# Optimization experiments

Measured on AMD Instinct MI355X. Metric: run time of the kernel, lower is better.

## Reference

```python
import jax, jax.numpy as jnp
import numpy as np

D = 512      # d_model
H = 8        # nhead
HD = D // H  # head dim
L = 8        # axis-0 length (torch seq dim, batch_first=False)
S = 128      # axis-1 length (torch batch dim; relation-tensor axis)
NL = 3       # encoder layers
EPS = 1e-5


def setup_inputs() -> dict:
    key = jax.random.key(0)
    ks = jax.random.split(key, 16)
    w = lambda k, shape: jax.random.normal(k, shape, jnp.float32) * 0.02
    return {
        "x": jax.random.normal(ks[0], (L, S, D), jnp.float32),
        # stacked per-layer transformer params (leading dim = NL)
        "attn_in_w": w(ks[1], (NL, 3 * D, D)), "attn_in_b": jnp.zeros((NL, 3 * D), jnp.float32),
        "attn_out_w": w(ks[2], (NL, D, D)),    "attn_out_b": jnp.zeros((NL, D), jnp.float32),
        "ln1_w": jnp.ones((NL, D), jnp.float32), "ln1_b": jnp.zeros((NL, D), jnp.float32),
        "ln2_w": jnp.ones((NL, D), jnp.float32), "ln2_b": jnp.zeros((NL, D), jnp.float32),
        "ff1_w": w(ks[3], (NL, 4 * D, D)), "ff1_b": jnp.zeros((NL, 4 * D), jnp.float32),
        "ff2_w": w(ks[4], (NL, D, 4 * D)), "ff2_b": jnp.zeros((NL, D), jnp.float32),
        "fln_w": jnp.ones((D,), jnp.float32), "fln_b": jnp.zeros((D,), jnp.float32),
        # 4 projection MLPs stacked: 0=sub, 1=obj, 2=verb_sub, 3=verb_obj
        "mlp_w0": w(ks[5], (4, D, D)), "mlp_b0": jnp.zeros((4, D), jnp.float32),
        "mlp_w1": w(ks[6], (4, D, D)), "mlp_b1": jnp.zeros((4, D), jnp.float32),
        "mlp_w2": w(ks[7], (4, D, D)), "mlp_b2": jnp.zeros((4, D), jnp.float32),
    }


def _ln(x, w, b):
    m = jnp.mean(x, axis=-1, keepdims=True)
    v = jnp.mean(jnp.square(x - m), axis=-1, keepdims=True)
    return (x - m) * jax.lax.rsqrt(v + EPS) * w + b


def _mha(x, in_w, in_b, out_w, out_b):
    # x: (L, B, D); attention over axis 0 (torch batch_first=False semantics)
    l, b, _ = x.shape
    qkv = x @ in_w.T + in_b                      # (L, B, 3D)
    q, k, v = jnp.split(qkv, 3, axis=-1)
    q = q.reshape(l, b, H, HD)
    k = k.reshape(l, b, H, HD)
    v = v.reshape(l, b, H, HD)
    scores = jnp.einsum("lbhd,mbhd->bhlm", q, k) / jnp.sqrt(jnp.float32(HD))
    attn = jax.nn.softmax(scores, axis=-1)
    o = jnp.einsum("bhlm,mbhd->lbhd", attn, v).reshape(l, b, D)
    return o @ out_w.T + out_b


def _mlp(x, w0, b0, w1, b1, w2, b2):
    h = jax.nn.relu(x @ w0.T + b0)
    h = jax.nn.relu(h @ w1.T + b1)
    return h @ w2.T + b2


def _forward(x, attn_in_w, attn_in_b, attn_out_w, attn_out_b,
             ln1_w, ln1_b, ln2_w, ln2_b, ff1_w, ff1_b, ff2_w, ff2_b,
             fln_w, fln_b, mlp_w0, mlp_b0, mlp_w1, mlp_b1, mlp_w2, mlp_b2):
    # TransformerEncoder (post-norm, relu, no dropout at eval)
    h = x
    for i in range(NL):
        h = _ln(h + _mha(h, attn_in_w[i], attn_in_b[i], attn_out_w[i], attn_out_b[i]),
                ln1_w[i], ln1_b[i])
        ff = jax.nn.relu(h @ ff1_w[i].T + ff1_b[i]) @ ff2_w[i].T + ff2_b[i]
        h = _ln(h + ff, ln2_w[i], ln2_b[i])
    h = _ln(h, fln_w, fln_b)  # final encoder norm

    sub = _mlp(h, mlp_w0[0], mlp_b0[0], mlp_w1[0], mlp_b1[0], mlp_w2[0], mlp_b2[0])
    obj = _mlp(h, mlp_w0[1], mlp_b0[1], mlp_w1[1], mlp_b1[1], mlp_w2[1], mlp_b2[1])
    vsub = _mlp(h, mlp_w0[2], mlp_b0[2], mlp_w1[2], mlp_b1[2], mlp_w2[2], mlp_b2[2])
    vobj = _mlp(h, mlp_w0[3], mlp_b0[3], mlp_w1[3], mlp_b1[3], mlp_w2[3], mlp_b2[3])

    # sub.unsqueeze(1) * vsub.unsqueeze(2): (B0, S, S, D)
    sub4 = sub[:, None, :, :] * vsub[:, :, None, :]
    obj4 = obj[:, None, :, :] * vobj[:, :, None, :]
    # p_x = sub4 @ obj4.transpose(-2, -1): (B0, S, S, S)
    return jnp.einsum("bijd,bikd->bijk", sub4, obj4)


def reference(x, attn_in_w, attn_in_b, attn_out_w, attn_out_b,
              ln1_w, ln1_b, ln2_w, ln2_b, ff1_w, ff1_b, ff2_w, ff2_b,
              fln_w, fln_b, mlp_w0, mlp_b0, mlp_w1, mlp_b1, mlp_w2, mlp_b2):
    return _forward(x, attn_in_w, attn_in_b, attn_out_w, attn_out_b,
                    ln1_w, ln1_b, ln2_w, ln2_b, ff1_w, ff1_b, ff2_w, ff2_b,
                    fln_w, fln_b, mlp_w0, mlp_b0, mlp_w1, mlp_b1, mlp_w2, mlp_b2)
```

## Files before the change

kernel.cpp:

```cpp
#include <hip/hip_runtime.h>
#include <hip/hip_bf16.h>

#define DEV __device__ __forceinline__

typedef __attribute__((ext_vector_type(8))) short bf16x8;
typedef __attribute__((ext_vector_type(8))) unsigned short u16x8;
typedef __attribute__((ext_vector_type(4))) float f32x4;

DEV unsigned short f2bf(float f) {
  return __builtin_bit_cast(unsigned short, __float2bfloat16(f));
}
DEV float bf2f(unsigned short h) { return __uint_as_float(((unsigned int)h) << 16); }

DEV int swz(int row, int byteoff) { return row * 128 + (byteoff ^ ((row & 7) << 4)); }

__global__ void cvt_kernel(const float* __restrict__ src, unsigned short* __restrict__ dst,
                           float* __restrict__ dstf, int n) {
  long i = ((long)blockIdx.x * blockDim.x + threadIdx.x) * 8;
  long stride = (long)gridDim.x * blockDim.x * 8;
  for (; i < n; i += stride) {
    f32x4 a = *(const f32x4*)(src + i);
    f32x4 b = *(const f32x4*)(src + i + 4);
    u16x8 o;
    o[0] = f2bf(a[0]); o[1] = f2bf(a[1]); o[2] = f2bf(a[2]); o[3] = f2bf(a[3]);
    o[4] = f2bf(b[0]); o[5] = f2bf(b[1]); o[6] = f2bf(b[2]); o[7] = f2bf(b[3]);
    *(u16x8*)(dst + i) = o;
    if (dstf) { *(f32x4*)(dstf + i) = a; *(f32x4*)(dstf + i + 4) = b; }
  }
}

struct CvtJobs { const float* s[7]; unsigned short* d[7]; int n[7]; };
__global__ void cvtw_kernel(CvtJobs J) {
  const int seg = blockIdx.y;
  const float* __restrict__ src = J.s[seg];
  unsigned short* __restrict__ dst = J.d[seg];
  const int n = J.n[seg];
  long i = ((long)blockIdx.x * blockDim.x + threadIdx.x) * 8;
  long stride = (long)gridDim.x * blockDim.x * 8;
  for (; i < n; i += stride) {
    f32x4 a = *(const f32x4*)(src + i);
    f32x4 b = *(const f32x4*)(src + i + 4);
    u16x8 o;
    o[0] = f2bf(a[0]); o[1] = f2bf(a[1]); o[2] = f2bf(a[2]); o[3] = f2bf(a[3]);
    o[4] = f2bf(b[0]); o[5] = f2bf(b[1]); o[6] = f2bf(b[2]); o[7] = f2bf(b[3]);
    *(u16x8*)(dst + i) = o;
  }
}

template <int BM, int ACT, int WF32, int WBF>
__global__ __launch_bounds__(256) void gemm_kernel(
    const unsigned short* __restrict__ X, const unsigned short* __restrict__ Wt,
    const float* __restrict__ bias, float* Yf, unsigned short* __restrict__ Ybf,
    int M, int N, int K, long xbs, long wbs, long bbs, long ybs) {
  constexpr int CA = (BM * 64) / (256 * 8);
  constexpr int ABY = BM * 64 * 2;
  constexpr int BBY = 64 * 64 * 2;
  constexpr int MI = BM / 32;
  __shared__ __align__(16) char Asb[2 * ABY];
  __shared__ __align__(16) char Bsb[2 * BBY];
  const int t = threadIdx.x;
  const int bn = blockIdx.x, bm = blockIdx.y, bz = blockIdx.z;
  const unsigned short* Xp = X + (long)bz * xbs;
  const unsigned short* Wp = Wt + (long)bz * wbs;

  const int lane = t & 63, wv = t >> 6;
  const int wr = wv >> 1, wc = wv & 1;
  f32x4 acc[MI][2] = {};

  int rowA[CA], slotA[CA], rowB[2], slotB[2];
#pragma unroll
  for (int c = 0; c < CA; ++c) { int id = c * 256 + t; rowA[c] = id >> 3; slotA[c] = id & 7; }
#pragma unroll
  for (int c = 0; c < 2; ++c) { int id = c * 256 + t; rowB[c] = id >> 3; slotB[c] = id & 7; }

  u16x8 ra[CA], rb[2];
  auto load = [&](int kt) {
#pragma unroll
    for (int c = 0; c < CA; ++c)
      ra[c] = *(const u16x8*)(Xp + (long)(bm * BM + rowA[c]) * K + kt + slotA[c] * 8);
#pragma unroll
    for (int c = 0; c < 2; ++c)
      rb[c] = *(const u16x8*)(Wp + (long)(bn * 64 + rowB[c]) * K + kt + slotB[c] * 8);
  };
  auto store = [&](int cur) {
#pragma unroll
    for (int c = 0; c < CA; ++c)
      *(u16x8*)(Asb + cur * ABY + swz(rowA[c], slotA[c] * 16)) = ra[c];
#pragma unroll
    for (int c = 0; c < 2; ++c)
      *(u16x8*)(Bsb + cur * BBY + swz(rowB[c], slotB[c] * 16)) = rb[c];
  };

  const int NT = K >> 6;
  load(0);
  store(0);
  load(64);
  __syncthreads();
  for (int ki = 0; ki < NT; ++ki) {
    const int cur = ki & 1;
    if (ki + 1 < NT) store(cur ^ 1);
    if (ki + 2 < NT) load((ki + 2) << 6);
#pragma unroll
    for (int kk = 0; kk < 2; ++kk) {
      const int kb = kk * 64 + ((lane >> 4) << 4);
      bf16x8 af[MI], bfv[2];
#pragma unroll
      for (int mi = 0; mi < MI; ++mi)
        af[mi] = *(const bf16x8*)(Asb + cur * ABY + swz(wr * (MI * 16) + mi * 16 + (lane & 15), kb));
#pragma unroll
      for (int ni = 0; ni < 2; ++ni)
        bfv[ni] = *(const bf16x8*)(Bsb + cur * BBY + swz(wc * 32 + ni * 16 + (lane & 15), kb));
#pragma unroll
      for (int mi = 0; mi < MI; ++mi)
#pragma unroll
        for (int ni = 0; ni < 2; ++ni)
          acc[mi][ni] = __builtin_amdgcn_mfma_f32_16x16x32_bf16(af[mi], bfv[ni], acc[mi][ni], 0, 0, 0);
    }
    __syncthreads();
  }
#pragma unroll
  for (int ni = 0; ni < 2; ++ni) {
    const int n = bn * 64 + wc * 32 + ni * 16 + (lane & 15);
    const float bv = bias[(long)bz * bbs + n];
#pragma unroll
    for (int mi = 0; mi < MI; ++mi) {
#pragma unroll
      for (int rr = 0; rr < 4; ++rr) {
        const int gm = bm * BM + wr * (MI * 16) + mi * 16 + ((lane >> 4) << 2) + rr;
        float v = acc[mi][ni][rr] + bv;
        if (ACT == 1) v = fmaxf(v, 0.f);
        const long o = (long)bz * ybs + (long)gm * N + n;
        if (WF32) Yf[o] = v;
        if (WBF) Ybf[o] = f2bf(v);
      }
    }
  }
}

__global__ __launch_bounds__(256) void attn_kernel(const unsigned short* __restrict__ qkv,
                                                   unsigned short* __restrict__ o) {
  __shared__ float P[512];
  const int s = blockIdx.x;
  const int t = threadIdx.x;
#pragma unroll
  for (int rep = 0; rep < 2; ++rep) {
    const int idx = t + rep * 256;
    const int h = idx >> 6, l = (idx >> 3) & 7, m = idx & 7;
    const unsigned short* qp = qkv + (long)(l * 128 + s) * 1536 + h * 64;
    const unsigned short* kp = qkv + (long)(m * 128 + s) * 1536 + 512 + h * 64;
    float acc = 0.f;
#pragma unroll
    for (int c = 0; c < 64; c += 8) {
      u16x8 q8 = *(const u16x8*)(qp + c);
      u16x8 k8 = *(const u16x8*)(kp + c);
#pragma unroll
      for (int j = 0; j < 8; ++j) acc += bf2f(q8[j]) * bf2f(k8[j]);
    }
    P[idx] = acc * 0.125f;
  }
  __syncthreads();
  if (t < 64) {
    const int base = t * 8;
    float mx = -1e30f;
#pragma unroll
    for (int m = 0; m < 8; ++m) mx = fmaxf(mx, P[base + m]);
    float e[8], sum = 0.f;
#pragma unroll
    for (int m = 0; m < 8; ++m) { e[m] = expf(P[base + m] - mx); sum += e[m]; }
    const float inv = 1.f / sum;
#pragma unroll
    for (int m = 0; m < 8; ++m) P[base + m] = e[m] * inv;
  }
  __syncthreads();
#pragma unroll
  for (int rep = 0; rep < 16; ++rep) {
    const int idx = t + rep * 256;
    const int d = idx & 63, h = (idx >> 6) & 7, l = idx >> 9;
    float acc = 0.f;
#pragma unroll
    for (int m = 0; m < 8; ++m)
      acc += P[h * 64 + l * 8 + m] * bf2f(qkv[(long)(m * 128 + s) * 1536 + 1024 + h * 64 + d]);
    o[(long)(l * 128 + s) * 512 + h * 64 + d] = f2bf(acc);
  }
}

template <int RES, int WF32>
__global__ __launch_bounds__(256) void ln_kernel(const float* a, const float* res,
                                                 const float* __restrict__ w,
                                                 const float* __restrict__ bb, float* hf,
                                                 unsigned short* __restrict__ hbf) {
  __shared__ float red[8];
  const int row = blockIdx.x, t = threadIdx.x;
  const long base = (long)row * 512;
  float x0 = a[base + t], x1 = a[base + t + 256];
  if (RES) { x0 += res[base + t]; x1 += res[base + t + 256]; }
  float s = x0 + x1;
#pragma unroll
  for (int msk = 32; msk; msk >>= 1) s += __shfl_xor(s, msk, 64);
  if ((t & 63) == 0) red[t >> 6] = s;
  __syncthreads();
  const float mean = (red[0] + red[1] + red[2] + red[3]) * (1.f / 512.f);
  const float d0 = x0 - mean, d1 = x1 - mean;
  float v = d0 * d0 + d1 * d1;
#pragma unroll
  for (int msk = 32; msk; msk >>= 1) v += __shfl_xor(v, msk, 64);
  if ((t & 63) == 0) red[4 + (t >> 6)] = v;
  __syncthreads();
  const float var = (red[4] + red[5] + red[6] + red[7]) * (1.f / 512.f);
  const float inv = rsqrtf(var + 1e-5f);
  const float o0 = d0 * inv * w[t] + bb[t];
  const float o1 = d1 * inv * w[t + 256] + bb[t + 256];
  if (WF32) { hf[base + t] = o0; hf[base + t + 256] = o1; }
  hbf[base + t] = f2bf(o0);
  hbf[base + t + 256] = f2bf(o1);
}

__global__ __launch_bounds__(256) void phasec_kernel(const float* __restrict__ subp,
                                                     const unsigned short* __restrict__ objbf,
                                                     const float* __restrict__ vsub,
                                                     const float* __restrict__ vobj,
                                                     float* __restrict__ out) {
  constexpr int ABY = 128 * 64 * 2;
  __shared__ __align__(16) char Asb[2 * ABY];
  __shared__ __align__(16) char Bsb[2 * ABY];
  __shared__ float Wl[512];
  const int t = threadIdx.x;
  const int i = blockIdx.x, b = blockIdx.y;
  const long base_bi = ((long)b * 128 + i) * 512;
  for (int d = t; d < 512; d += 256) Wl[d] = vsub[base_bi + d] * vobj[base_bi + d];

  const int lane = t & 63, wv = t >> 6;
  const int wr = wv >> 1, wc = wv & 1;
  f32x4 acc[4][4] = {};

  int row[4], slot[4];
#pragma unroll
  for (int c = 0; c < 4; ++c) { int id = c * 256 + t; row[c] = id >> 3; slot[c] = id & 7; }

  f32x4 fa[4][2];
  u16x8 rb[4];
  auto load = [&](int kt) {
#pragma unroll
    for (int c = 0; c < 4; ++c) {
      const long g = ((long)b * 128 + row[c]) * 512 + kt + slot[c] * 8;
      fa[c][0] = *(const f32x4*)(subp + g);
      fa[c][1] = *(const f32x4*)(subp + g + 4);
      rb[c] = *(const u16x8*)(objbf + g);
    }
  };
  auto store = [&](int cur, int ktd) {
#pragma unroll
    for (int c = 0; c < 4; ++c) {
      const float* wp = Wl + ktd + slot[c] * 8;
      f32x4 w0 = *(const f32x4*)wp;
      f32x4 w1 = *(const f32x4*)(wp + 4);
      u16x8 oa;
      oa[0] = f2bf(fa[c][0][0] * w0[0]); oa[1] = f2bf(fa[c][0][1] * w0[1]);
      oa[2] = f2bf(fa[c][0][2] * w0[2]); oa[3] = f2bf(fa[c][0][3] * w0[3]);
      oa[4] = f2bf(fa[c][1][0] * w1[0]); oa[5] = f2bf(fa[c][1][1] * w1[1]);
      oa[6] = f2bf(fa[c][1][2] * w1[2]); oa[7] = f2bf(fa[c][1][3] * w1[3]);
      *(u16x8*)(Asb + cur * ABY + swz(row[c], slot[c] * 16)) = oa;
      *(u16x8*)(Bsb + cur * ABY + swz(row[c], slot[c] * 16)) = rb[c];
    }
  };

  __syncthreads();
  load(0);
  store(0, 0);
  load(64);
  __syncthreads();
  for (int ki = 0; ki < 8; ++ki) {
    const int cur = ki & 1;
    if (ki + 1 < 8) store(cur ^ 1, (ki + 1) * 64);
    if (ki + 2 < 8) load((ki + 2) * 64);
#pragma unroll
    for (int kk = 0; kk < 2; ++kk) {
      const int kb = kk * 64 + ((lane >> 4) << 4);
      bf16x8 af[4], bfv[4];
#pragma unroll
      for (int mi = 0; mi < 4; ++mi)
        af[mi] = *(const bf16x8*)(Asb + cur * ABY + swz(wr * 64 + mi * 16 + (lane & 15), kb));
#pragma unroll
      for (int ni = 0; ni < 4; ++ni)
        bfv[ni] = *(const bf16x8*)(Bsb + cur * ABY + swz(wc * 64 + ni * 16 + (lane & 15), kb));
#pragma unroll
      for (int mi = 0; mi < 4; ++mi)
#pragma unroll
        for (int ni = 0; ni < 4; ++ni)
          acc[mi][ni] = __builtin_amdgcn_mfma_f32_16x16x32_bf16(af[mi], bfv[ni], acc[mi][ni], 0, 0, 0);
    }
    __syncthreads();
  }
  float* ob = out + ((long)b * 128 + i) * 128 * 128;
#pragma unroll
  for (int mi = 0; mi < 4; ++mi) {
#pragma unroll
    for (int rr = 0; rr < 4; ++rr) {
      const int j = wr * 64 + mi * 16 + ((lane >> 4) << 2) + rr;
      float* orow = ob + (long)j * 128 + wc * 64 + (lane & 15);
#pragma unroll
      for (int ni = 0; ni < 4; ++ni) orow[ni * 16] = acc[mi][ni][rr];
    }
  }
}

extern "C" void kernel_launch(void* const* d_in, const int* in_sizes, int n_in, void* d_out,
                              int out_size, void* d_ws, size_t ws_size, hipStream_t stream) {
  const float* x          = (const float*)d_in[0];
  const float* attn_in_w  = (const float*)d_in[1];
  const float* attn_in_b  = (const float*)d_in[2];
  const float* attn_out_w = (const float*)d_in[3];
  const float* attn_out_b = (const float*)d_in[4];
  const float* ln1_w = (const float*)d_in[5];
  const float* ln1_b = (const float*)d_in[6];
  const float* ln2_w = (const float*)d_in[7];
  const float* ln2_b = (const float*)d_in[8];
  const float* ff1_w = (const float*)d_in[9];
  const float* ff1_b = (const float*)d_in[10];
  const float* ff2_w = (const float*)d_in[11];
  const float* ff2_b = (const float*)d_in[12];
  const float* fln_w = (const float*)d_in[13];
  const float* fln_b = (const float*)d_in[14];
  const float* mlp_w0 = (const float*)d_in[15];
  const float* mlp_b0 = (const float*)d_in[16];
  const float* mlp_w1 = (const float*)d_in[17];
  const float* mlp_b1 = (const float*)d_in[18];
  const float* mlp_w2 = (const float*)d_in[19];
  const float* mlp_b2 = (const float*)d_in[20];
  float* out = (float*)d_out;
  (void)in_sizes; (void)n_in; (void)out_size; (void)ws_size;

  char* ws = (char*)d_ws;
  size_t off = 0;
  auto alloc = [&](size_t bytes) -> void* {
    void* p = (void*)(ws + off);
    off += (bytes + 255) & ~(size_t)255;
    return p;
  };
  unsigned short* wq  = (unsigned short*)alloc((size_t)3 * 1536 * 512 * 2);
  unsigned short* wo  = (unsigned short*)alloc((size_t)3 * 512 * 512 * 2);
  unsigned short* wf1 = (unsigned short*)alloc((size_t)3 * 2048 * 512 * 2);
  unsigned short* wf2 = (unsigned short*)alloc((size_t)3 * 512 * 2048 * 2);
  unsigned short* wm0 = (unsigned short*)alloc((size_t)4 * 512 * 512 * 2);
  unsigned short* wm1 = (unsigned short*)alloc((size_t)4 * 512 * 512 * 2);
  unsigned short* wm2 = (unsigned short*)alloc((size_t)4 * 512 * 512 * 2);
  float* h            = (float*)alloc((size_t)1024 * 512 * 4);
  unsigned short* hbf = (unsigned short*)alloc((size_t)1024 * 512 * 2);
  unsigned short* t1  = (unsigned short*)alloc((size_t)1024 * 2048 * 2);
  float* t2           = (float*)alloc((size_t)1024 * 512 * 4);
  unsigned short* ao  = (unsigned short*)alloc((size_t)1024 * 512 * 2);
  unsigned short* z1  = (unsigned short*)alloc((size_t)4 * 1024 * 512 * 2);
  unsigned short* z2  = (unsigned short*)alloc((size_t)4 * 1024 * 512 * 2);
  float* hf4          = (float*)alloc((size_t)4 * 1024 * 512 * 4);
  unsigned short* hb4 = (unsigned short*)alloc((size_t)4 * 1024 * 512 * 2);

  CvtJobs J;
  J.s[0] = attn_in_w;  J.d[0] = wq;  J.n[0] = 3 * 1536 * 512;
  J.s[1] = attn_out_w; J.d[1] = wo;  J.n[1] = 3 * 512 * 512;
  J.s[2] = ff1_w;      J.d[2] = wf1; J.n[2] = 3 * 2048 * 512;
  J.s[3] = ff2_w;      J.d[3] = wf2; J.n[3] = 3 * 512 * 2048;
  J.s[4] = mlp_w0;     J.d[4] = wm0; J.n[4] = 4 * 512 * 512;
  J.s[5] = mlp_w1;     J.d[5] = wm1; J.n[5] = 4 * 512 * 512;
  J.s[6] = mlp_w2;     J.d[6] = wm2; J.n[6] = 4 * 512 * 512;
  cvtw_kernel<<<dim3(512, 7), 256, 0, stream>>>(J);
  cvt_kernel<<<256, 256, 0, stream>>>(x, hbf, h, 1024 * 512);

  for (int i = 0; i < 3; ++i) {
    gemm_kernel<64, 0, 0, 1><<<dim3(24, 16, 1), 256, 0, stream>>>(
        hbf, wq + (long)i * 1536 * 512, attn_in_b + i * 1536, nullptr, t1, 1024, 1536, 512, 0, 0, 0, 0);
    attn_kernel<<<128, 256, 0, stream>>>(t1, ao);
    gemm_kernel<32, 0, 1, 0><<<dim3(8, 32, 1), 256, 0, stream>>>(
        ao, wo + (long)i * 512 * 512, attn_out_b + i * 512, t2, nullptr, 1024, 512, 512, 0, 0, 0, 0);
    ln_kernel<1, 1><<<1024, 256, 0, stream>>>(t2, h, ln1_w + i * 512, ln1_b + i * 512, h, hbf);
    gemm_kernel<64, 1, 0, 1><<<dim3(32, 16, 1), 256, 0, stream>>>(
        hbf, wf1 + (long)i * 2048 * 512, ff1_b + i * 2048, nullptr, t1, 1024, 2048, 512, 0, 0, 0, 0);
    gemm_kernel<32, 0, 1, 0><<<dim3(8, 32, 1), 256, 0, stream>>>(
        t1, wf2 + (long)i * 512 * 2048, ff2_b + i * 512, t2, nullptr, 1024, 512, 2048, 0, 0, 0, 0);
    ln_kernel<1, 1><<<1024, 256, 0, stream>>>(t2, h, ln2_w + i * 512, ln2_b + i * 512, h, hbf);
  }
  ln_kernel<0, 0><<<1024, 256, 0, stream>>>(h, nullptr, fln_w, fln_b, h, hbf);

  gemm_kernel<32, 1, 0, 1><<<dim3(8, 32, 4), 256, 0, stream>>>(
      hbf, wm0, mlp_b0, nullptr, z1, 1024, 512, 512, 0, 512 * 512, 512, 1024 * 512);
  gemm_kernel<32, 1, 0, 1><<<dim3(8, 32, 4), 256, 0, stream>>>(
      z1, wm1, mlp_b1, nullptr, z2, 1024, 512, 512, 1024 * 512, 512 * 512, 512, 1024 * 512);
  gemm_kernel<32, 0, 1, 1><<<dim3(8, 32, 4), 256, 0, stream>>>(
      z2, wm2, mlp_b2, hf4, hb4, 1024, 512, 512, 1024 * 512, 512 * 512, 512, 1024 * 512);

  phasec_kernel<<<dim3(128, 8), 256, 0, stream>>>(
      hf4, hb4 + 1 * 1024 * 512, hf4 + 2L * 1024 * 512, hf4 + 3L * 1024 * 512, out);
}
```

Baseline: 379.6 us.

## Fuse LayerNorms into GEMM prologue/epilogue via atomic row statistics

Removes the standalone LayerNorm kernels. GEMM epilogues now add the residual, accumulate per-row sum and sum-of-squares with atomics, and the next GEMM applies the normalization while loading its fp32 A tile. The change also widens GEMM tiles to 64x128 for the wide projections, folds the input conversion into the batched weight-convert launch, and stages the phase-C output through LDS for coalesced vector stores. The cost is a single-pass variance (E[x^2]-mean^2) with atomic accumulation, a memset, fp32 A-operand loads, and renormalizing the residual redundantly in epilogues.

```diff
diff --git a/kernel.cpp b/kernel.cpp
--- a/kernel.cpp
+++ b/kernel.cpp
@@ -14,22 +14,7 @@
 
 DEV int swz(int row, int byteoff) { return row * 128 + (byteoff ^ ((row & 7) << 4)); }
 
-__global__ void cvt_kernel(const float* __restrict__ src, unsigned short* __restrict__ dst,
-                           float* __restrict__ dstf, int n) {
-  long i = ((long)blockIdx.x * blockDim.x + threadIdx.x) * 8;
-  long stride = (long)gridDim.x * blockDim.x * 8;
-  for (; i < n; i += stride) {
-    f32x4 a = *(const f32x4*)(src + i);
-    f32x4 b = *(const f32x4*)(src + i + 4);
-    u16x8 o;
-    o[0] = f2bf(a[0]); o[1] = f2bf(a[1]); o[2] = f2bf(a[2]); o[3] = f2bf(a[3]);
-    o[4] = f2bf(b[0]); o[5] = f2bf(b[1]); o[6] = f2bf(b[2]); o[7] = f2bf(b[3]);
-    *(u16x8*)(dst + i) = o;
-    if (dstf) { *(f32x4*)(dstf + i) = a; *(f32x4*)(dstf + i + 4) = b; }
-  }
-}
-
-struct CvtJobs { const float* s[7]; unsigned short* d[7]; int n[7]; };
+struct CvtJobs { const float* s[8]; unsigned short* d[8]; int n[8]; };
 __global__ void cvtw_kernel(CvtJobs J) {
   const int seg = blockIdx.y;
   const float* __restrict__ src = J.s[seg];
@@ -47,91 +32,151 @@
   }
 }
 
-template <int BM, int ACT, int WF32, int WBF>
-__global__ __launch_bounds__(256) void gemm_kernel(
-    const unsigned short* __restrict__ X, const unsigned short* __restrict__ Wt,
-    const float* __restrict__ bias, float* Yf, unsigned short* __restrict__ Ybf,
+template <int BM, int BN, int ALN, int RES, int RLN, int ACT, int STATS, int OUTF32, int OUTBF>
+__global__ __launch_bounds__(256) void gemm2_kernel(
+    const unsigned short* __restrict__ Xb, const float* __restrict__ Xf,
+    const float* __restrict__ sA, const float* __restrict__ gA, const float* __restrict__ bA,
+    const unsigned short* __restrict__ W, const float* __restrict__ bias,
+    const float* __restrict__ resf, const float* __restrict__ sR,
+    const float* __restrict__ gR, const float* __restrict__ bR,
+    float* __restrict__ Yf, unsigned short* __restrict__ Ybf, float* __restrict__ stats,
     int M, int N, int K, long xbs, long wbs, long bbs, long ybs) {
-  constexpr int CA = (BM * 64) / (256 * 8);
-  constexpr int ABY = BM * 64 * 2;
-  constexpr int BBY = 64 * 64 * 2;
-  constexpr int MI = BM / 32;
+  constexpr int CA = BM / 32, CB = BN / 32;
+  constexpr int ABY = BM * 64 * 2, BBY = BN * 64 * 2;
+  constexpr int MI = BM / 32, NI = BN / 32;
   __shared__ __align__(16) char Asb[2 * ABY];
   __shared__ __align__(16) char Bsb[2 * BBY];
   const int t = threadIdx.x;
   const int bn = blockIdx.x, bm = blockIdx.y, bz = blockIdx.z;
-  const unsigned short* Xp = X + (long)bz * xbs;
-  const unsigned short* Wp = Wt + (long)bz * wbs;
-
-  const int lane = t & 63, wv = t >> 6;
-  const int wr = wv >> 1, wc = wv & 1;
-  f32x4 acc[MI][2] = {};
-
-  int rowA[CA], slotA[CA], rowB[2], slotB[2];
+  const int lane = t & 63, wv = t >> 6, wr = wv >> 1, wc = wv & 1;
+
+  int rowA[CA], slotA[CA], rowB[CB], slotB[CB];
 #pragma unroll
   for (int c = 0; c < CA; ++c) { int id = c * 256 + t; rowA[c] = id >> 3; slotA[c] = id & 7; }
 #pragma unroll
-  for (int c = 0; c < 2; ++c) { int id = c * 256 + t; rowB[c] = id >> 3; slotB[c] = id & 7; }
-
-  u16x8 ra[CA], rb[2];
+  for (int c = 0; c < CB; ++c) { int id = c * 256 + t; rowB[c] = id >> 3; slotB[c] = id & 7; }
+
+  float mA[CA], iA[CA];
+  if (ALN) {
+#pragma unroll
+    for (int c = 0; c < CA; ++c) {
+      const int gm = bm * BM + rowA[c];
+      const float s = sA[2 * gm], q = sA[2 * gm + 1];
+      mA[c] = s * (1.f / 512.f);
+      iA[c] = rsqrtf(q * (1.f / 512.f) - mA[c] * mA[c] + 1e-5f);
+    }
+  }
+
+  f32x4 acc[MI][NI];
+#pragma unroll
+  for (int mi = 0; mi < MI; ++mi)
+#pragma unroll
+    for (int ni = 0; ni < NI; ++ni) acc[mi][ni] = f32x4{0.f, 0.f, 0.f, 0.f};
+
+  u16x8 ra[CA], rb[CB];
+  f32x4 raf[CA][2];
   auto load = [&](int kt) {
 #pragma unroll
-    for (int c = 0; c < CA; ++c)
-      ra[c] = *(const u16x8*)(Xp + (long)(bm * BM + rowA[c]) * K + kt + slotA[c] * 8);
-#pragma unroll
-    for (int c = 0; c < 2; ++c)
-      rb[c] = *(const u16x8*)(Wp + (long)(bn * 64 + rowB[c]) * K + kt + slotB[c] * 8);
+    for (int c = 0; c < CA; ++c) {
+      if (ALN) {
+        const float* p = Xf + (long)(bm * BM + rowA[c]) * K + kt + slotA[c] * 8;
+        raf[c][0] = *(const f32x4*)p;
+        raf[c][1] = *(const f32x4*)(p + 4);
+      } else {
+        ra[c] = *(const u16x8*)(Xb + (long)bz * xbs + (long)(bm * BM + rowA[c]) * K + kt + slotA[c] * 8);
+      }
+    }
+#pragma unroll
+    for (int c = 0; c < CB; ++c)
+      rb[c] = *(const u16x8*)(W + (long)bz * wbs + (long)(bn * BN + rowB[c]) * K + kt + slotB[c] * 8);
   };
-  auto store = [&](int cur) {
-#pragma unroll
-    for (int c = 0; c < CA; ++c)
-      *(u16x8*)(Asb + cur * ABY + swz(rowA[c], slotA[c] * 16)) = ra[c];
-#pragma unroll
-    for (int c = 0; c < 2; ++c)
+  auto store = [&](int cur, int kt) {
+#pragma unroll
+    for (int c = 0; c < CA; ++c) {
+      if (ALN) {
+        const int col = kt + slotA[c] * 8;
+        f32x4 g0 = *(const f32x4*)(gA + col), g1 = *(const f32x4*)(gA + col + 4);
+        f32x4 b0 = *(const f32x4*)(bA + col), b1 = *(const f32x4*)(bA + col + 4);
+        u16x8 o;
+#pragma unroll
+        for (int j = 0; j < 4; ++j) o[j] = f2bf((raf[c][0][j] - mA[c]) * iA[c] * g0[j] + b0[j]);
+#pragma unroll
+        for (int j = 0; j < 4; ++j) o[4 + j] = f2bf((raf[c][1][j] - mA[c]) * iA[c] * g1[j] + b1[j]);
+        *(u16x8*)(Asb + cur * ABY + swz(rowA[c], slotA[c] * 16)) = o;
+      } else {
+        *(u16x8*)(Asb + cur * ABY + swz(rowA[c], slotA[c] * 16)) = ra[c];
+      }
+    }
+#pragma unroll
+    for (int c = 0; c < CB; ++c)
       *(u16x8*)(Bsb + cur * BBY + swz(rowB[c], slotB[c] * 16)) = rb[c];
   };
 
   const int NT = K >> 6;
   load(0);
-  store(0);
+  store(0, 0);
   load(64);
   __syncthreads();
   for (int ki = 0; ki < NT; ++ki) {
     const int cur = ki & 1;
-    if (ki + 1 < NT) store(cur ^ 1);
+    if (ki + 1 < NT) store(cur ^ 1, (ki + 1) << 6);
     if (ki + 2 < NT) load((ki + 2) << 6);
 #pragma unroll
     for (int kk = 0; kk < 2; ++kk) {
       const int kb = kk * 64 + ((lane >> 4) << 4);
-      bf16x8 af[MI], bfv[2];
+      bf16x8 af[MI], bfv[NI];
 #pragma unroll
       for (int mi = 0; mi < MI; ++mi)
-        af[mi] = *(const bf16x8*)(Asb + cur * ABY + swz(wr * (MI * 16) + mi * 16 + (lane & 15), kb));
-#pragma unroll
-      for (int ni = 0; ni < 2; ++ni)
-        bfv[ni] = *(const bf16x8*)(Bsb + cur * BBY + swz(wc * 32 + ni * 16 + (lane & 15), kb));
+        af[mi] = *(const bf16x8*)(Asb + cur * ABY + swz(wr * (BM / 2) + mi * 16 + (lane & 15), kb));
+#pragma unroll
+      for (int ni = 0; ni < NI; ++ni)
+        bfv[ni] = *(const bf16x8*)(Bsb + cur * BBY + swz(wc * (BN / 2) + ni * 16 + (lane & 15), kb));
 #pragma unroll
       for (int mi = 0; mi < MI; ++mi)
 #pragma unroll
-        for (int ni = 0; ni < 2; ++ni)
+        for (int ni = 0; ni < NI; ++ni)
           acc[mi][ni] = __builtin_amdgcn_mfma_f32_16x16x32_bf16(af[mi], bfv[ni], acc[mi][ni], 0, 0, 0);
     }
     __syncthreads();
   }
-#pragma unroll
-  for (int ni = 0; ni < 2; ++ni) {
-    const int n = bn * 64 + wc * 32 + ni * 16 + (lane & 15);
-    const float bv = bias[(long)bz * bbs + n];
-#pragma unroll
-    for (int mi = 0; mi < MI; ++mi) {
-#pragma unroll
-      for (int rr = 0; rr < 4; ++rr) {
-        const int gm = bm * BM + wr * (MI * 16) + mi * 16 + ((lane >> 4) << 2) + rr;
-        float v = acc[mi][ni][rr] + bv;
-        if (ACT == 1) v = fmaxf(v, 0.f);
-        const long o = (long)bz * ybs + (long)gm * N + n;
-        if (WF32) Yf[o] = v;
-        if (WBF) Ybf[o] = f2bf(v);
+
+#pragma unroll
+  for (int mi = 0; mi < MI; ++mi) {
+#pragma unroll
+    for (int rr = 0; rr < 4; ++rr) {
+      const int gm = bm * BM + wr * (BM / 2) + mi * 16 + ((lane >> 4) << 2) + rr;
+      float mR, iR;
+      if (RES && RLN) {
+        const float s = sR[2 * gm], q = sR[2 * gm + 1];
+        mR = s * (1.f / 512.f);
+        iR = rsqrtf(q * (1.f / 512.f) - mR * mR + 1e-5f);
+      }
+      float srow = 0.f, qrow = 0.f;
+#pragma unroll
+      for (int ni = 0; ni < NI; ++ni) {
+        const int gn = bn * BN + wc * (BN / 2) + ni * 16 + (lane & 15);
+        float v = acc[mi][ni][rr] + bias[(long)bz * bbs + gn];
+        if (RES) {
+          float r = resf[(long)gm * 512 + gn];
+          if (RLN) r = (r - mR) * iR * gR[gn] + bR[gn];
+          v += r;
+        }
+        if (ACT) v = fmaxf(v, 0.f);
+        if (STATS) { srow += v; qrow += v * v; }
+        const long o = (long)bz * ybs + (long)gm * N + gn;
+        if (OUTF32) Yf[o] = v;
+        if (OUTBF) Ybf[o] = f2bf(v);
+      }
+      if (STATS) {
+#pragma unroll
+        for (int msk = 1; msk < 16; msk <<= 1) {
+          srow += __shfl_xor(srow, msk, 64);
+          qrow += __shfl_xor(qrow, msk, 64);
+        }
+        if ((lane & 15) == 0) {
+          atomicAdd(&stats[2 * gm], srow);
+          atomicAdd(&stats[2 * gm + 1], qrow);
+        }
       }
     }
   }
@@ -184,35 +229,41 @@
   }
 }
 
-template <int RES, int WF32>
-__global__ __launch_bounds__(256) void ln_kernel(const float* a, const float* res,
-                                                 const float* __restrict__ w,
-                                                 const float* __restrict__ bb, float* hf,
-                                                 unsigned short* __restrict__ hbf) {
-  __shared__ float red[8];
-  const int row = blockIdx.x, t = threadIdx.x;
-  const long base = (long)row * 512;
-  float x0 = a[base + t], x1 = a[base + t + 256];
-  if (RES) { x0 += res[base + t]; x1 += res[base + t + 256]; }
-  float s = x0 + x1;
-#pragma unroll
-  for (int msk = 32; msk; msk >>= 1) s += __shfl_xor(s, msk, 64);
-  if ((t & 63) == 0) red[t >> 6] = s;
-  __syncthreads();
-  const float mean = (red[0] + red[1] + red[2] + red[3]) * (1.f / 512.f);
-  const float d0 = x0 - mean, d1 = x1 - mean;
-  float v = d0 * d0 + d1 * d1;
-#pragma unroll
-  for (int msk = 32; msk; msk >>= 1) v += __shfl_xor(v, msk, 64);
-  if ((t & 63) == 0) red[4 + (t >> 6)] = v;
-  __syncthreads();
-  const float var = (red[4] + red[5] + red[6] + red[7]) * (1.f / 512.f);
-  const float inv = rsqrtf(var + 1e-5f);
-  const float o0 = d0 * inv * w[t] + bb[t];
-  const float o1 = d1 * inv * w[t + 256] + bb[t + 256];
-  if (WF32) { hf[base + t] = o0; hf[base + t + 256] = o1; }
-  hbf[base + t] = f2bf(o0);
-  hbf[base + t + 256] = f2bf(o1);
+__global__ __launch_bounds__(256) void lastln_kernel(const float* __restrict__ t2,
+                                                     const float* __restrict__ S,
+                                                     const float* __restrict__ g2,
+                                                     const float* __restrict__ b2,
+                                                     const float* __restrict__ gf,
+                                                     const float* __restrict__ bf_,
+                                                     unsigned short* __restrict__ out) {
+  const int t = threadIdx.x, lane = t & 63, wv = t >> 6;
+  const int row = blockIdx.x * 4 + wv;
+  const float* p = t2 + (long)row * 512 + lane * 8;
+  f32x4 a = *(const f32x4*)p;
+  f32x4 c = *(const f32x4*)(p + 4);
+  const float s0 = S[2 * row], q0 = S[2 * row + 1];
+  const float m1 = s0 * (1.f / 512.f);
+  const float i1 = rsqrtf(q0 * (1.f / 512.f) - m1 * m1 + 1e-5f);
+  float v[8];
+  const float* g2p = g2 + lane * 8;
+  const float* b2p = b2 + lane * 8;
+#pragma unroll
+  for (int j = 0; j < 4; ++j) v[j] = (a[j] - m1) * i1 * g2p[j] + b2p[j];
+#pragma unroll
+  for (int j = 0; j < 4; ++j) v[4 + j] = (c[j] - m1) * i1 * g2p[4 + j] + b2p[4 + j];
+  float s = 0.f, q = 0.f;
+#pragma unroll
+  for (int j = 0; j < 8; ++j) { s += v[j]; q += v[j] * v[j]; }
+#pragma unroll
+  for (int msk = 32; msk; msk >>= 1) { s += __shfl_xor(s, msk, 64); q += __shfl_xor(q, msk, 64); }
+  const float m2 = s * (1.f / 512.f);
+  const float i2 = rsqrtf(q * (1.f / 512.f) - m2 * m2 + 1e-5f);
+  const float* gfp = gf + lane * 8;
+  const float* bfp = bf_ + lane * 8;
+  u16x8 o;
+#pragma unroll
+  for (int j = 0; j < 8; ++j) o[j] = f2bf((v[j] - m2) * i2 * gfp[j] + bfp[j]);
+  *(u16x8*)(out + (long)row * 512 + lane * 8) = o;
 }
 
 __global__ __launch_bounds__(256) void phasec_kernel(const float* __restrict__ subp,
@@ -221,9 +272,10 @@
                                                      const float* __restrict__ vobj,
                                                      float* __restrict__ out) {
   constexpr int ABY = 128 * 64 * 2;
-  __shared__ __align__(16) char Asb[2 * ABY];
-  __shared__ __align__(16) char Bsb[2 * ABY];
-  __shared__ float Wl[512];
+  __shared__ __align__(16) char SMEM[67584];
+  char* Asb = SMEM;
+  char* Bsb = SMEM + 2 * ABY;
+  float* Wl = (float*)(SMEM + 4 * ABY);
   const int t = threadIdx.x;
   const int i = blockIdx.x, b = blockIdx.y;
   const long base_bi = ((long)b * 128 + i) * 512;
@@ -291,16 +343,24 @@
     }
     __syncthreads();
   }
-  float* ob = out + ((long)b * 128 + i) * 128 * 128;
-#pragma unroll
-  for (int mi = 0; mi < 4; ++mi) {
+  float* C = (float*)SMEM;
+#pragma unroll
+  for (int mi = 0; mi < 4; ++mi)
 #pragma unroll
     for (int rr = 0; rr < 4; ++rr) {
       const int j = wr * 64 + mi * 16 + ((lane >> 4) << 2) + rr;
-      float* orow = ob + (long)j * 128 + wc * 64 + (lane & 15);
-#pragma unroll
-      for (int ni = 0; ni < 4; ++ni) orow[ni * 16] = acc[mi][ni][rr];
-    }
+      float* crow = C + j * 132 + wc * 64 + (lane & 15);
+#pragma unroll
+      for (int ni = 0; ni < 4; ++ni) crow[ni * 16] = acc[mi][ni][rr];
+    }
+  __syncthreads();
+  float* ob = out + ((long)b * 128 + i) * 128 * 128;
+  const int cc = (t & 31) * 4, jb = (t >> 5) * 16;
+#pragma unroll
+  for (int q = 0; q < 16; ++q) {
+    const int j = jb + q;
+    f32x4 v = *(const f32x4*)(C + j * 132 + cc);
+    *(f32x4*)(ob + (long)j * 128 + cc) = v;
   }
 }
 
@@ -337,6 +397,7 @@
     off += (bytes + 255) & ~(size_t)255;
     return p;
   };
+  float* stats        = (float*)alloc((size_t)6 * 1024 * 2 * 4);
   unsigned short* wq  = (unsigned short*)alloc((size_t)3 * 1536 * 512 * 2);
   unsigned short* wo  = (unsigned short*)alloc((size_t)3 * 512 * 512 * 2);
   unsigned short* wf1 = (unsigned short*)alloc((size_t)3 * 2048 * 512 * 2);
@@ -344,15 +405,18 @@
   unsigned short* wm0 = (unsigned short*)alloc((size_t)4 * 512 * 512 * 2);
   unsigned short* wm1 = (unsigned short*)alloc((size_t)4 * 512 * 512 * 2);
   unsigned short* wm2 = (unsigned short*)alloc((size_t)4 * 512 * 512 * 2);
-  float* h            = (float*)alloc((size_t)1024 * 512 * 4);
-  unsigned short* hbf = (unsigned short*)alloc((size_t)1024 * 512 * 2);
+  unsigned short* hbf0 = (unsigned short*)alloc((size_t)1024 * 512 * 2);
   unsigned short* t1  = (unsigned short*)alloc((size_t)1024 * 2048 * 2);
-  float* t2           = (float*)alloc((size_t)1024 * 512 * 4);
   unsigned short* ao  = (unsigned short*)alloc((size_t)1024 * 512 * 2);
+  float* t2a          = (float*)alloc((size_t)1024 * 512 * 4);
+  float* t2b          = (float*)alloc((size_t)1024 * 512 * 4);
+  unsigned short* hbfH = (unsigned short*)alloc((size_t)1024 * 512 * 2);
   unsigned short* z1  = (unsigned short*)alloc((size_t)4 * 1024 * 512 * 2);
   unsigned short* z2  = (unsigned short*)alloc((size_t)4 * 1024 * 512 * 2);
   float* hf4          = (float*)alloc((size_t)4 * 1024 * 512 * 4);
   unsigned short* hb4 = (unsigned short*)alloc((size_t)4 * 1024 * 512 * 2);
+
+  hipMemsetAsync(stats, 0, (size_t)6 * 1024 * 2 * 4, stream);
 
   CvtJobs J;
   J.s[0] = attn_in_w;  J.d[0] = wq;  J.n[0] = 3 * 1536 * 512;
@@ -362,30 +426,52 @@
   J.s[4] = mlp_w0;     J.d[4] = wm0; J.n[4] = 4 * 512 * 512;
   J.s[5] = mlp_w1;     J.d[5] = wm1; J.n[5] = 4 * 512 * 512;
   J.s[6] = mlp_w2;     J.d[6] = wm2; J.n[6] = 4 * 512 * 512;
-  cvtw_kernel<<<dim3(512, 7), 256, 0, stream>>>(J);
-  cvt_kernel<<<256, 256, 0, stream>>>(x, hbf, h, 1024 * 512);
-
-  for (int i = 0; i < 3; ++i) {
-    gemm_kernel<64, 0, 0, 1><<<dim3(24, 16, 1), 256, 0, stream>>>(
-        hbf, wq + (long)i * 1536 * 512, attn_in_b + i * 1536, nullptr, t1, 1024, 1536, 512, 0, 0, 0, 0);
+  J.s[7] = x;          J.d[7] = hbf0; J.n[7] = 1024 * 512;
+  cvtw_kernel<<<dim3(512, 8), 256, 0, stream>>>(J);
+
+  for (int L = 0; L < 3; ++L) {
+    float* Sout = stats + (2 * L) * 2048;
+    float* Sff  = stats + (2 * L + 1) * 2048;
+    const float* Sprev = stats + (2 * L - 1) * 2048;
+    if (L == 0)
+      gemm2_kernel<64, 128, 0, 0, 0, 0, 0, 0, 1><<<dim3(12, 16), 256, 0, stream>>>(
+          hbf0, nullptr, nullptr, nullptr, nullptr, wq, attn_in_b, nullptr, nullptr, nullptr,
+          nullptr, nullptr, t1, nullptr, 1024, 1536, 512, 0, 0, 0, 0);
+    else
+      gemm2_kernel<64, 128, 1, 0, 0, 0, 0, 0, 1><<<dim3(12, 16), 256, 0, stream>>>(
+          nullptr, t2b, Sprev, ln2_w + (L - 1) * 512, ln2_b + (L - 1) * 512,
+          wq + (long)L * 1536 * 512, attn_in_b + L * 1536, nullptr, nullptr, nullptr,
+          nullptr, nullptr, t1, nullptr, 1024, 1536, 512, 0, 0, 0, 0);
     attn_kernel<<<128, 256, 0, stream>>>(t1, ao);
-    gemm_kernel<32, 0, 1, 0><<<dim3(8, 32, 1), 256, 0, stream>>>(
-        ao, wo + (long)i * 512 * 512, attn_out_b + i * 512, t2, nullptr, 1024, 512, 512, 0, 0, 0, 0);
-    ln_kernel<1, 1><<<1024, 256, 0, stream>>>(t2, h, ln1_w + i * 512, ln1_b + i * 512, h, hbf);
-    gemm_kernel<64, 1, 0, 1><<<dim3(32, 16, 1), 256, 0, stream>>>(
-        hbf, wf1 + (long)i * 2048 * 512, ff1_b + i * 2048, nullptr, t1, 1024, 2048, 512, 0, 0, 0, 0);
-    gemm_kernel<32, 0, 1, 0><<<dim3(8, 32, 1), 256, 0, stream>>>(
-        t1, wf2 + (long)i * 512 * 2048, ff2_b + i * 512, t2, nullptr, 1024, 512, 2048, 0, 0, 0, 0);
-    ln_kernel<1, 1><<<1024, 256, 0, stream>>>(t2, h, ln2_w + i * 512, ln2_b + i * 512, h, hbf);
-  }
-  ln_kernel<0, 0><<<1024, 256, 0, stream>>>(h, nullptr, fln_w, fln_b, h, hbf);
-
-  gemm_kernel<32, 1, 0, 1><<<dim3(8, 32, 4), 256, 0, stream>>>(
-      hbf, wm0, mlp_b0, nullptr, z1, 1024, 512, 512, 0, 512 * 512, 512, 1024 * 512);
-  gemm_kernel<32, 1, 0, 1><<<dim3(8, 32, 4), 256, 0, stream>>>(
-      z1, wm1, mlp_b1, nullptr, z2, 1024, 512, 512, 1024 * 512, 512 * 512, 512, 1024 * 512);
-  gemm_kernel<32, 0, 1, 1><<<dim3(8, 32, 4), 256, 0, stream>>>(
-      z2, wm2, mlp_b2, hf4, hb4, 1024, 512, 512, 1024 * 512, 512 * 512, 512, 1024 * 512);
+    if (L == 0)
+      gemm2_kernel<32, 64, 0, 1, 0, 0, 1, 1, 0><<<dim3(8, 32), 256, 0, stream>>>(
+          ao, nullptr, nullptr, nullptr, nullptr, wo, attn_out_b, x, nullptr, nullptr, nullptr,
+          t2a, nullptr, Sout, 1024, 512, 512, 0, 0, 0, 0);
+    else
+      gemm2_kernel<32, 64, 0, 1, 1, 0, 1, 1, 0><<<dim3(8, 32), 256, 0, stream>>>(
+          ao, nullptr, nullptr, nullptr, nullptr, wo + (long)L * 512 * 512, attn_out_b + L * 512,
+          t2b, Sprev, ln2_w + (L - 1) * 512, ln2_b + (L - 1) * 512,
+          t2a, nullptr, Sout, 1024, 512, 512, 0, 0, 0, 0);
+    gemm2_kernel<64, 128, 1, 0, 0, 1, 0, 0, 1><<<dim3(16, 16), 256, 0, stream>>>(
+        nullptr, t2a, Sout, ln1_w + L * 512, ln1_b + L * 512,
+        wf1 + (long)L * 2048 * 512, ff1_b + L * 2048, nullptr, nullptr, nullptr, nullptr,
+        nullptr, t1, nullptr, 1024, 2048, 512, 0, 0, 0, 0);
+    gemm2_kernel<32, 64, 0, 1, 1, 0, 1, 1, 0><<<dim3(8, 32), 256, 0, stream>>>(
+        t1, nullptr, nullptr, nullptr, nullptr, wf2 + (long)L * 512 * 2048, ff2_b + L * 512,
+        t2a, Sout, ln1_w + L * 512, ln1_b + L * 512,
+        t2b, nullptr, Sff, 1024, 512, 2048, 0, 0, 0, 0);
+  }
+  lastln_kernel<<<256, 256, 0, stream>>>(t2b, stats + 5 * 2048, ln2_w + 2 * 512, ln2_b + 2 * 512,
+                                         fln_w, fln_b, hbfH);
+  gemm2_kernel<64, 128, 0, 0, 0, 1, 0, 0, 1><<<dim3(4, 16, 4), 256, 0, stream>>>(
+      hbfH, nullptr, nullptr, nullptr, nullptr, wm0, mlp_b0, nullptr, nullptr, nullptr, nullptr,
+      nullptr, z1, nullptr, 1024, 512, 512, 0, 512 * 512, 512, 1024 * 512);
+  gemm2_kernel<64, 128, 0, 0, 0, 1, 0, 0, 1><<<dim3(4, 16, 4), 256, 0, stream>>>(
+      z1, nullptr, nullptr, nullptr, nullptr, wm1, mlp_b1, nullptr, nullptr, nullptr, nullptr,
+      nullptr, z2, nullptr, 1024, 512, 512, 1024 * 512, 512 * 512, 512, 1024 * 512);
+  gemm2_kernel<64, 128, 0, 0, 0, 0, 0, 1, 1><<<dim3(4, 16, 4), 256, 0, stream>>>(
+      z2, nullptr, nullptr, nullptr, nullptr, wm2, mlp_b2, nullptr, nullptr, nullptr, nullptr,
+      hf4, hb4, nullptr, 1024, 512, 512, 1024 * 512, 512 * 512, 512, 1024 * 512);
 
   phasec_kernel<<<dim3(128, 8), 256, 0, stream>>>(
       hf4, hb4 + 1 * 1024 * 512, hf4 + 2L * 1024 * 512, hf4 + 3L * 1024 * 512, out);
```

Measured after the change: 388.8 us. +2.4%, slower.
